# Kernel tuning notes

Hardware: AMD Instinct MI355X
Metric: run time of the kernel (lower is better)

The kernel has to match this reference:

```python
import jax, jax.numpy as jnp
import numpy as np


def setup_inputs() -> dict:
    key = jax.random.key(0)
    ks = jax.random.split(key, 8)
    B, L, E = 4096, 200, 64
    H1, H2 = 80, 40
    q = jax.random.normal(ks[0], (B, 1, E), dtype=jnp.float32)
    k = jax.random.normal(ks[1], (B, L, E), dtype=jnp.float32)
    v = jax.random.normal(ks[2], (B, L, E), dtype=jnp.float32)
    mask = jax.random.randint(ks[3], (B, L, 1), 0, 2).astype(bool)
    # Linear weights stored as [in, out] (torch stores [out, in]; math identical)
    W1 = jax.random.normal(ks[4], (4 * E, H1), dtype=jnp.float32) * 0.05
    b1 = jnp.zeros((H1,), dtype=jnp.float32)
    W2 = jax.random.normal(ks[5], (H1, H2), dtype=jnp.float32) * 0.05
    b2 = jnp.zeros((H2,), dtype=jnp.float32)
    Wf = jax.random.normal(ks[6], (H2, 1), dtype=jnp.float32) * 0.05
    bf = jnp.zeros((1,), dtype=jnp.float32)
    return {"q": q, "k": k, "v": v, "mask": mask,
            "W1": W1, "b1": b1, "W2": W2, "b2": b2, "Wf": Wf, "bf": bf}


def reference(q, k, v, mask, W1, b1, W2, b2, Wf, bf):
    # q: [B,1,E] broadcast to [B,L,E]
    qr = jnp.broadcast_to(q, k.shape)
    info = jnp.concatenate([qr, k, qr - k, qr * k], axis=-1)  # [B,L,4E]
    info = info @ W1 + b1                                      # [B,L,H1]
    info = info @ W2 + b2                                      # [B,L,H2]
    info = jax.nn.sigmoid(info)  # single sigmoid after the dense stack, as in source
    logits = info @ Wf + bf                                    # [B,L,1]
    logits = jnp.where(mask, -jnp.inf, logits)
    score = jax.nn.softmax(logits, axis=1)                     # softmax over history dim
    # score^T @ v -> [B,1,E] -> squeeze
    out = jnp.einsum('bl,ble->be', score[..., 0], v)
    return out
```

## Files before the change

### kernel.cpp

```cpp
#include <hip/hip_runtime.h>
#include <hip/hip_bf16.h>
#include <math.h>

namespace {

constexpr int L   = 200;
constexpr int E   = 64;
constexpr int H1N = 80;
constexpr int H2N = 40;

using short8 = __attribute__((ext_vector_type(8))) short;
using f32x4  = __attribute__((ext_vector_type(4))) float;

__device__ inline unsigned short f2bu(float f) {
    return (unsigned short)__builtin_bit_cast(short, __float2bfloat16(f));
}

#define ROR_ADD(x, CTRL) do {                                                   \
    int _t = __builtin_amdgcn_update_dpp(0, __builtin_bit_cast(int, (x)),       \
                                         (CTRL), 0xf, 0xf, true);               \
    (x) += __builtin_bit_cast(float, _t); } while (0)

constexpr int WS_AF   = 0;
constexpr int WS_CF   = 20480;
constexpr int WS_W2F  = 40960;
constexpr int WS_FLAG = 50176;
constexpr int WS_CQ   = 50432;

__global__ void k0_prep(const float* __restrict__ W1,
                        const float* __restrict__ W2,
                        const float* __restrict__ q,
                        const float* __restrict__ b1,
                        const void* __restrict__ mask,
                        float* __restrict__ Af,
                        float* __restrict__ Cf,
                        unsigned short* __restrict__ W2f,
                        float* __restrict__ cq_all,
                        int* __restrict__ flagG, int B)
{
    const int id = blockIdx.x * 256 + threadIdx.x;
    if (id < 640) {
        const int u  = id, cc = u >> 6, ln = u & 63;
        const int nt = cc >> 1, ks = cc & 1;
        const int j  = nt * 16 + (ln & 15);
        const int i0 = ks * 32 + (ln >> 4) * 8;
        #pragma unroll
        for (int e = 0; e < 8; ++e) {
            const int i = i0 + e;
            Af[u * 8 + e] = W1[(E + i) * H1N + j] - W1[(2 * E + i) * H1N + j];
            Cf[u * 8 + e] = W1[(3 * E + i) * H1N + j];
        }
    } else if (id < 1216) {
        const int u   = id - 640, cc = u >> 6, ln = u & 63;
        const int nt2 = cc / 3, ks2 = cc % 3;
        const int n   = nt2 * 16 + (ln & 15);
        const int j0  = ks2 * 32 + (ln >> 4) * 8;
        #pragma unroll
        for (int e = 0; e < 8; ++e) {
            const int j = j0 + e;
            W2f[u * 8 + e] = (j < H1N && n < H2N) ? f2bu(W2[j * H2N + n])
                                                  : (unsigned short)0;
        }
    } else {
        const int t = id - 1216;
        if (t > B * 20) return;
        if (t == B * 20) {
            const unsigned char* mb = (const unsigned char*)mask;
            int isI32 = 1;
            for (int i = 0; i < 256; ++i)
                if ((i & 3) && mb[i]) { isI32 = 0; break; }
            flagG[0] = isI32;
            return;
        }
        const int b  = t / 20;
        const int jq = (t - b * 20) * 4;
        const float* qb = q + (size_t)b * E;
        float4 a = *(const float4*)(b1 + jq);
        #pragma unroll 8
        for (int i = 0; i < E; ++i) {
            const float qv = qb[i];
            const float4 wa = *(const float4*)(W1 + i * H1N + jq);
            const float4 wb = *(const float4*)(W1 + (2 * E + i) * H1N + jq);
            a.x += qv * (wa.x + wb.x);
            a.y += qv * (wa.y + wb.y);
            a.z += qv * (wa.z + wb.z);
            a.w += qv * (wa.w + wb.w);
        }
        *(float4*)(cq_all + (size_t)b * H1N + jq) = a;
    }
}

__global__ __launch_bounds__(256, 6)
void attn_main(const float* __restrict__ q,
               const float* __restrict__ kmat,
               const float* __restrict__ vmat,
               const void* __restrict__ mask,
               const float* __restrict__ b2,
               const float* __restrict__ Wf,
               const float* __restrict__ bfp,
               const float* __restrict__ Af,
               const float* __restrict__ Cf,
               const unsigned short* __restrict__ W2fG,
               const float* __restrict__ cq_all,
               const int* __restrict__ flagG,
               float* __restrict__ out)
{
    const int tid  = threadIdx.x;
    const int lane = tid & 63;
    const int wv   = tid >> 6;
    const int g    = lane >> 4;
    const int c    = lane & 15;

    __shared__ short8 Mt[640];
    __shared__ unsigned short H1t[4][16][104];
    __shared__ float score[256];
    __shared__ float part_s[4][64];
    __shared__ float red_s[8];

    const int bb = blockIdx.x;

    *(unsigned long long*)&H1t[wv][c][80 + g * 4] = 0ULL;

    const float* qbase = q + (size_t)bb * E;
    for (int u = tid; u < 640; u += 256) {
        const int cc = u >> 6, ln = u & 63;
        const int i0 = (cc & 1) * 32 + (ln >> 4) * 8;
        const float4 a0 = *(const float4*)(Af + u * 8);
        const float4 a1 = *(const float4*)(Af + u * 8 + 4);
        const float4 c0 = *(const float4*)(Cf + u * 8);
        const float4 c1 = *(const float4*)(Cf + u * 8 + 4);
        const float4 q0 = *(const float4*)(qbase + i0);
        const float4 q1 = *(const float4*)(qbase + i0 + 4);
        short8 h;
        h[0] = (short)f2bu(a0.x + q0.x * c0.x);
        h[1] = (short)f2bu(a0.y + q0.y * c0.y);
        h[2] = (short)f2bu(a0.z + q0.z * c0.z);
        h[3] = (short)f2bu(a0.w + q0.w * c0.w);
        h[4] = (short)f2bu(a1.x + q1.x * c1.x);
        h[5] = (short)f2bu(a1.y + q1.y * c1.y);
        h[6] = (short)f2bu(a1.z + q1.z * c1.z);
        h[7] = (short)f2bu(a1.w + q1.w * c1.w);
        Mt[u] = h;
    }

    float cqr[5];
    #pragma unroll
    for (int nt = 0; nt < 5; ++nt)
        cqr[nt] = cq_all[(size_t)bb * H1N + nt * 16 + c];
    float b2r[3], wfr[3];
    #pragma unroll
    for (int nt2 = 0; nt2 < 3; ++nt2) {
        const int nc = nt2 * 16 + c;
        b2r[nt2] = (nc < H2N) ? b2[nc] : 0.f;
        wfr[nt2] = (nc < H2N) ? Wf[nc] : 0.f;
    }
    const float bf0 = bfp[0];
    const short8* W2v = (const short8*)W2fG;
    const float*  kbase = kmat + (size_t)bb * (L * E);
    __syncthreads();

    #pragma unroll 1
    for (int rt = 0; rt < 4; ++rt) {
        const int t = wv + 4 * rt;
        if (t < 13) {
            const float4* kp = (const float4*)(kbase + (size_t)min(16 * t + c, L - 1) * E);
            const float4 kb0 = kp[2 * g];
            const float4 kb1 = kp[2 * g + 1];
            const float4 kb2 = kp[8 + 2 * g];
            const float4 kb3 = kp[8 + 2 * g + 1];

            short8 ak0, ak1;
            ak0[0] = (short)f2bu(kb0.x); ak0[1] = (short)f2bu(kb0.y);
            ak0[2] = (short)f2bu(kb0.z); ak0[3] = (short)f2bu(kb0.w);
            ak0[4] = (short)f2bu(kb1.x); ak0[5] = (short)f2bu(kb1.y);
            ak0[6] = (short)f2bu(kb1.z); ak0[7] = (short)f2bu(kb1.w);
            ak1[0] = (short)f2bu(kb2.x); ak1[1] = (short)f2bu(kb2.y);
            ak1[2] = (short)f2bu(kb2.z); ak1[3] = (short)f2bu(kb2.w);
            ak1[4] = (short)f2bu(kb3.x); ak1[5] = (short)f2bu(kb3.y);
            ak1[6] = (short)f2bu(kb3.z); ak1[7] = (short)f2bu(kb3.w);

            f32x4 acc1[5];
            #pragma unroll
            for (int nt = 0; nt < 5; ++nt) acc1[nt] = f32x4{0.f, 0.f, 0.f, 0.f};
            #pragma unroll
            for (int nt = 0; nt < 5; ++nt) {
                acc1[nt] = __builtin_amdgcn_mfma_f32_16x16x32_bf16(ak0, Mt[(nt * 2 + 0) * 64 + lane], acc1[nt], 0, 0, 0);
                acc1[nt] = __builtin_amdgcn_mfma_f32_16x16x32_bf16(ak1, Mt[(nt * 2 + 1) * 64 + lane], acc1[nt], 0, 0, 0);
            }

            #pragma unroll
            for (int nt = 0; nt < 5; ++nt)
                #pragma unroll
                for (int r = 0; r < 4; ++r)
                    H1t[wv][4 * g + r][nt * 16 + c] = f2bu(acc1[nt][r] + cqr[nt]);

            f32x4 acc2[3];
            #pragma unroll
            for (int nt2 = 0; nt2 < 3; ++nt2) acc2[nt2] = f32x4{0.f, 0.f, 0.f, 0.f};
            #pragma unroll
            for (int ks2 = 0; ks2 < 3; ++ks2) {
                const short8 a2 = *(const short8*)&H1t[wv][c][ks2 * 32 + g * 8];
                #pragma unroll
                for (int nt2 = 0; nt2 < 3; ++nt2)
                    acc2[nt2] = __builtin_amdgcn_mfma_f32_16x16x32_bf16(a2, W2v[(nt2 * 3 + ks2) * 64 + lane], acc2[nt2], 0, 0, 0);
            }

            float pl0 = 0.f, pl1 = 0.f, pl2 = 0.f, pl3 = 0.f;
            #pragma unroll
            for (int nt2 = 0; nt2 < 3; ++nt2) {
                const float wfv = wfr[nt2], b2v = b2r[nt2];
                pl0 += wfv * __builtin_amdgcn_rcpf(1.f + __expf(-(acc2[nt2][0] + b2v)));
                pl1 += wfv * __builtin_amdgcn_rcpf(1.f + __expf(-(acc2[nt2][1] + b2v)));
                pl2 += wfv * __builtin_amdgcn_rcpf(1.f + __expf(-(acc2[nt2][2] + b2v)));
                pl3 += wfv * __builtin_amdgcn_rcpf(1.f + __expf(-(acc2[nt2][3] + b2v)));
            }
            ROR_ADD(pl0, 0x128); ROR_ADD(pl0, 0x124); ROR_ADD(pl0, 0x122); ROR_ADD(pl0, 0x121);
            ROR_ADD(pl1, 0x128); ROR_ADD(pl1, 0x124); ROR_ADD(pl1, 0x122); ROR_ADD(pl1, 0x121);
            ROR_ADD(pl2, 0x128); ROR_ADD(pl2, 0x124); ROR_ADD(pl2, 0x122); ROR_ADD(pl2, 0x121);
            ROR_ADD(pl3, 0x128); ROR_ADD(pl3, 0x124); ROR_ADD(pl3, 0x122); ROR_ADD(pl3, 0x121);
            const float myv = (c == 0) ? pl0 : (c == 1) ? pl1 : (c == 2) ? pl2 : pl3;
            if (c < 4) score[16 * t + 4 * g + c] = bf0 + myv;
        }
    }
    __syncthreads();

    const int flagv = flagG[0];
    float logit = -INFINITY;
    if (tid < L) {
        logit = score[tid];
        const size_t mi = (size_t)bb * L + tid;
        const int mv = flagv ? ((const int*)mask)[mi]
                             : (int)((const unsigned char*)mask)[mi];
        if (mv != 0) logit = -INFINITY;
    }
    float m = logit;
    #pragma unroll
    for (int off = 32; off > 0; off >>= 1)
        m = fmaxf(m, __shfl_xor(m, off));
    if (lane == 0) red_s[wv] = m;
    __syncthreads();
    const float gmax = fmaxf(fmaxf(red_s[0], red_s[1]), fmaxf(red_s[2], red_s[3]));

    const float e = __expf(logit - gmax);
    score[tid] = e;
    float ssum = e;
    #pragma unroll
    for (int off = 32; off > 0; off >>= 1)
        ssum += __shfl_xor(ssum, off);
    if (lane == 0) red_s[4 + wv] = ssum;
    __syncthreads();
    const float inv = 1.0f / (red_s[4] + red_s[5] + red_s[6] + red_s[7]);

    f32x4 oa = f32x4{0.f, 0.f, 0.f, 0.f};
    const float* vb = vmat + (size_t)bb * (L * E);
    #pragma unroll
    for (int ll = 0; ll < 13; ++ll) {
        const int row = 16 * ll + 4 * wv + g;
        if (row < L) {
            const float sv = score[row];
            const float4 v4 = *(const float4*)(vb + (size_t)row * E + c * 4);
            oa[0] += sv * v4.x; oa[1] += sv * v4.y;
            oa[2] += sv * v4.z; oa[3] += sv * v4.w;
        }
    }
    #pragma unroll
    for (int j = 0; j < 4; ++j) {
        oa[j] += __shfl_xor(oa[j], 16);
        oa[j] += __shfl_xor(oa[j], 32);
    }
    if (g == 0)
        *(float4*)&part_s[wv][4 * c] = make_float4(oa[0], oa[1], oa[2], oa[3]);
    __syncthreads();
    if (tid < 64) {
        const float o = (part_s[0][tid] + part_s[1][tid]
                       + part_s[2][tid] + part_s[3][tid]) * inv;
        out[(size_t)bb * E + tid] = o;
    }
}

}

extern "C" void kernel_launch(void* const* d_in, const int* in_sizes, int n_in,
                              void* d_out, int out_size, void* d_ws, size_t ws_size,
                              hipStream_t stream) {
    const float* q  = (const float*)d_in[0];
    const float* k  = (const float*)d_in[1];
    const float* v  = (const float*)d_in[2];
    const void*  mk = d_in[3];
    const float* W1 = (const float*)d_in[4];
    const float* b1 = (const float*)d_in[5];
    const float* W2 = (const float*)d_in[6];
    const float* b2 = (const float*)d_in[7];
    const float* Wf = (const float*)d_in[8];
    const float* bf = (const float*)d_in[9];
    float* out = (float*)d_out;

    const int B = in_sizes[0] / E;

    char* ws = (char*)d_ws;
    float*          Af     = (float*)(ws + WS_AF);
    float*          Cf     = (float*)(ws + WS_CF);
    unsigned short* W2f    = (unsigned short*)(ws + WS_W2F);
    int*            flagG  = (int*)(ws + WS_FLAG);
    float*          cq_all = (float*)(ws + WS_CQ);

    const int prep_ids = 1216 + B * 20 + 1;
    k0_prep<<<(prep_ids + 255) / 256, 256, 0, stream>>>(W1, W2, q, b1, mk,
                                                        Af, Cf, W2f, cq_all, flagG, B);
    attn_main<<<B, 256, 0, stream>>>(q, k, v, mk, b2, Wf, bf,
                                     Af, Cf, W2f, cq_all, flagG, out);
}
```

Before: 124.0 us.

## Fuse softmax and PV accumulation into the MLP loop with 8 waves per block

Doubles the block to 512 threads so each wave handles at most two 16-row tiles. Exponentiated logits and the weighted V sum are now accumulated per wave inside the score loop, and the V rows are loaded early to overlap with the second MFMA stage. The max-subtraction pass and two block barriers are dropped, on the assumption that sigmoid-bounded logits cannot overflow exp. The risks are register pressure under the tighter launch bounds and reduced numerical safety for large Wf values.

Result: no change. 125.1 us (+0.9%).

```diff
diff --git a/kernel.cpp b/kernel.cpp
--- a/kernel.cpp
+++ b/kernel.cpp
@@ -90,7 +90,7 @@
     }
 }
 
-__global__ __launch_bounds__(256, 6)
+__global__ __launch_bounds__(512, 6)
 void attn_main(const float* __restrict__ q,
                const float* __restrict__ kmat,
                const float* __restrict__ vmat,
@@ -112,17 +112,17 @@
     const int c    = lane & 15;
 
     __shared__ short8 Mt[640];
-    __shared__ unsigned short H1t[4][16][104];
-    __shared__ float score[256];
-    __shared__ float part_s[4][64];
-    __shared__ float red_s[8];
+    __shared__ unsigned short H1t[8][16][104];
+    __shared__ float sc[8][16];
+    __shared__ float comb_p[8][64];
+    __shared__ float comb_s[8];
 
     const int bb = blockIdx.x;
 
     *(unsigned long long*)&H1t[wv][c][80 + g * 4] = 0ULL;
 
     const float* qbase = q + (size_t)bb * E;
-    for (int u = tid; u < 640; u += 256) {
+    for (int u = tid; u < 640; u += 512) {
         const int cc = u >> 6, ln = u & 63;
         const int i0 = (cc & 1) * 32 + (ln >> 4) * 8;
         const float4 a0 = *(const float4*)(Af + u * 8);
@@ -143,6 +143,7 @@
         Mt[u] = h;
     }
 
+    const int flagv = flagG[0];
     float cqr[5];
     #pragma unroll
     for (int nt = 0; nt < 5; ++nt)
@@ -157,13 +158,18 @@
     const float bf0 = bfp[0];
     const short8* W2v = (const short8*)W2fG;
     const float*  kbase = kmat + (size_t)bb * (L * E);
+    const float*  vb    = vmat + (size_t)bb * (L * E);
     __syncthreads();
 
-    #pragma unroll 1
-    for (int rt = 0; rt < 4; ++rt) {
-        const int t = wv + 4 * rt;
+    float s_w = 0.f;
+    f32x4 oa = f32x4{0.f, 0.f, 0.f, 0.f};
+
+    #pragma unroll
+    for (int rt = 0; rt < 2; ++rt) {
+        const int t = wv + 8 * rt;
         if (t < 13) {
-            const float4* kp = (const float4*)(kbase + (size_t)min(16 * t + c, L - 1) * E);
+            const int row0 = 16 * t;
+            const float4* kp = (const float4*)(kbase + (size_t)min(row0 + c, L - 1) * E);
             const float4 kb0 = kp[2 * g];
             const float4 kb1 = kp[2 * g + 1];
             const float4 kb2 = kp[8 + 2 * g];
@@ -193,6 +199,11 @@
                 #pragma unroll
                 for (int r = 0; r < 4; ++r)
                     H1t[wv][4 * g + r][nt * 16 + c] = f2bu(acc1[nt][r] + cqr[nt]);
+
+            const float4 v0 = *(const float4*)(vb + (size_t)min(row0 + 0 + g, L - 1) * E + c * 4);
+            const float4 v1 = *(const float4*)(vb + (size_t)min(row0 + 4 + g, L - 1) * E + c * 4);
+            const float4 v2 = *(const float4*)(vb + (size_t)min(row0 + 8 + g, L - 1) * E + c * 4);
+            const float4 v3 = *(const float4*)(vb + (size_t)min(row0 + 12 + g, L - 1) * E + c * 4);
 
             f32x4 acc2[3];
             #pragma unroll
@@ -218,63 +229,55 @@
             ROR_ADD(pl1, 0x128); ROR_ADD(pl1, 0x124); ROR_ADD(pl1, 0x122); ROR_ADD(pl1, 0x121);
             ROR_ADD(pl2, 0x128); ROR_ADD(pl2, 0x124); ROR_ADD(pl2, 0x122); ROR_ADD(pl2, 0x121);
             ROR_ADD(pl3, 0x128); ROR_ADD(pl3, 0x124); ROR_ADD(pl3, 0x122); ROR_ADD(pl3, 0x121);
-            const float myv = (c == 0) ? pl0 : (c == 1) ? pl1 : (c == 2) ? pl2 : pl3;
-            if (c < 4) score[16 * t + 4 * g + c] = bf0 + myv;
-        }
-    }
-    __syncthreads();
-
-    const int flagv = flagG[0];
-    float logit = -INFINITY;
-    if (tid < L) {
-        logit = score[tid];
-        const size_t mi = (size_t)bb * L + tid;
-        const int mv = flagv ? ((const int*)mask)[mi]
-                             : (int)((const unsigned char*)mask)[mi];
-        if (mv != 0) logit = -INFINITY;
-    }
-    float m = logit;
-    #pragma unroll
-    for (int off = 32; off > 0; off >>= 1)
-        m = fmaxf(m, __shfl_xor(m, off));
-    if (lane == 0) red_s[wv] = m;
-    __syncthreads();
-    const float gmax = fmaxf(fmaxf(red_s[0], red_s[1]), fmaxf(red_s[2], red_s[3]));
-
-    const float e = __expf(logit - gmax);
-    score[tid] = e;
-    float ssum = e;
-    #pragma unroll
-    for (int off = 32; off > 0; off >>= 1)
-        ssum += __shfl_xor(ssum, off);
-    if (lane == 0) red_s[4 + wv] = ssum;
-    __syncthreads();
-    const float inv = 1.0f / (red_s[4] + red_s[5] + red_s[6] + red_s[7]);
-
-    f32x4 oa = f32x4{0.f, 0.f, 0.f, 0.f};
-    const float* vb = vmat + (size_t)bb * (L * E);
-    #pragma unroll
-    for (int ll = 0; ll < 13; ++ll) {
-        const int row = 16 * ll + 4 * wv + g;
-        if (row < L) {
-            const float sv = score[row];
-            const float4 v4 = *(const float4*)(vb + (size_t)row * E + c * 4);
-            oa[0] += sv * v4.x; oa[1] += sv * v4.y;
-            oa[2] += sv * v4.z; oa[3] += sv * v4.w;
-        }
-    }
+
+            float p = 0.f;
+            const int rowi = row0 + 4 * g + c;
+            if (c < 4) {
+                if (rowi < L) {
+                    const float myv = (c == 0) ? pl0 : (c == 1) ? pl1 : (c == 2) ? pl2 : pl3;
+                    const size_t mi = (size_t)bb * L + rowi;
+                    const int mv = flagv ? ((const int*)mask)[mi]
+                                         : (int)((const unsigned char*)mask)[mi];
+                    if (!mv) p = __expf(bf0 + myv);
+                }
+                sc[wv][4 * g + c] = p;
+            }
+            float ps = p;
+            #pragma unroll
+            for (int off = 1; off < 64; off <<= 1)
+                ps += __shfl_xor(ps, off);
+            s_w += ps;
+
+            const float p0 = sc[wv][0 + g];
+            const float p1 = sc[wv][4 + g];
+            const float p2 = sc[wv][8 + g];
+            const float p3 = sc[wv][12 + g];
+            oa[0] += p0 * v0.x + p1 * v1.x + p2 * v2.x + p3 * v3.x;
+            oa[1] += p0 * v0.y + p1 * v1.y + p2 * v2.y + p3 * v3.y;
+            oa[2] += p0 * v0.z + p1 * v1.z + p2 * v2.z + p3 * v3.z;
+            oa[3] += p0 * v0.w + p1 * v1.w + p2 * v2.w + p3 * v3.w;
+        }
+    }
+
     #pragma unroll
     for (int j = 0; j < 4; ++j) {
         oa[j] += __shfl_xor(oa[j], 16);
         oa[j] += __shfl_xor(oa[j], 32);
     }
-    if (g == 0)
-        *(float4*)&part_s[wv][4 * c] = make_float4(oa[0], oa[1], oa[2], oa[3]);
+    if (lane < 16)
+        *(float4*)&comb_p[wv][4 * lane] = make_float4(oa[0], oa[1], oa[2], oa[3]);
+    if (lane == 0) comb_s[wv] = s_w;
     __syncthreads();
+
     if (tid < 64) {
-        const float o = (part_s[0][tid] + part_s[1][tid]
-                       + part_s[2][tid] + part_s[3][tid]) * inv;
-        out[(size_t)bb * E + tid] = o;
+        float den = comb_s[0];
+        float num = comb_p[0][tid];
+        #pragma unroll
+        for (int w = 1; w < 8; ++w) {
+            den += comb_s[w];
+            num += comb_p[w][tid];
+        }
+        out[(size_t)bb * E + tid] = num / den;
     }
 }
 
@@ -307,6 +310,6 @@
     const int prep_ids = 1216 + B * 20 + 1;
     k0_prep<<<(prep_ids + 255) / 256, 256, 0, stream>>>(W1, W2, q, b1, mk,
                                                         Af, Cf, W2f, cq_all, flagG, B);
-    attn_main<<<B, 256, 0, stream>>>(q, k, v, mk, b2, Wf, bf,
+    attn_main<<<B, 512, 0, stream>>>(q, k, v, mk, b2, Wf, bf,
                                      Af, Cf, W2f, cq_all, flagG, out);
 }
```
